# Optimization experiments

Hardware: AMD Instinct MI355X
Metric: run time of the kernel (lower is better)

Reference implementation:

```python
import jax, jax.numpy as jnp
import numpy as np

N, C, H, W = 8, 256, 128, 128
HD = 256          # hidden_depth
FC, FS, CS = 8, 2, 8  # heads_count, fold_size, center_size
EPS_GN = 1e-5


def setup_inputs() -> dict:
    key = jax.random.key(0)
    ks = jax.random.split(key, 8)
    d = {
        'x': jax.random.normal(ks[0], (N, C, H, W), jnp.float32),
        'proj_w': jax.random.normal(ks[1], (2 * HD, C), jnp.float32) * 0.02,
        'proj_b': jnp.zeros((2 * HD,), jnp.float32),
        'merge_w': jax.random.normal(ks[2], (C, HD), jnp.float32) * 0.02,
        'merge_b': jnp.zeros((C,), jnp.float32),
        'alpha': jnp.ones((1,), jnp.float32),
        'beta': jnp.zeros((1,), jnp.float32),
        'g0_w': jnp.ones((C,), jnp.float32),
        'g0_b': jnp.zeros((C,), jnp.float32),
        'mlp_w0': jax.random.normal(ks[3], (2 * C, 2 * C), jnp.float32) * 0.02,
        'mlp_b0': jnp.zeros((2 * C,), jnp.float32),
        'mlp_w1': jax.random.normal(ks[4], (2 * C, C), jnp.float32) * 0.02,
        'mlp_b1': jnp.zeros((C,), jnp.float32),
        'g1_w': jnp.ones((C,), jnp.float32),
        'g1_b': jnp.zeros((C,), jnp.float32),
        'layer_scale': jnp.full((C,), 1e-5, jnp.float32),
    }
    return d


def _group_norm1(x, w, b):
    # GroupNorm(1, C): normalize over (C,H,W) per sample, per-channel affine
    mu = x.mean(axis=(1, 2, 3), keepdims=True)
    var = ((x - mu) ** 2).mean(axis=(1, 2, 3), keepdims=True)
    xn = (x - mu) * jax.lax.rsqrt(var + EPS_GN)
    return xn * w[None, :, None, None] + b[None, :, None, None]


def _l2norm(v):
    return v / jnp.maximum(jnp.linalg.norm(v, axis=-1, keepdims=True), 1e-12)


def _local_cluster(x, proj_w, proj_b, merge_w, merge_b, alpha, beta):
    n = x.shape[0]
    # 1x1 conv proj: C -> 2*HD
    y = jnp.einsum('nchw,oc->nohw', x, proj_w) + proj_b[None, :, None, None]
    c = y.shape[1] // FC              # per-head channels (2*HD/FC)
    h, w = H // FS, W // FS
    # 'n (fc c) (fh h) (fw w) -> (n fc fh fw) c h w'
    y = y.reshape(n, FC, c, FS, h, FS, w).transpose(0, 1, 3, 5, 2, 4, 6)
    y = y.reshape(n * FC * FS * FS, c, h, w)
    m = y.shape[0]
    # adaptive avg pool to CSxCS (h,w divisible by CS -> uniform pooling)
    center = y.reshape(m, c, CS, h // CS, CS, w // CS).mean(axis=(3, 5))
    L, s = h * w, CS * CS
    yf = y.reshape(m, c, L).transpose(0, 2, 1)       # [m, L, c]
    cf = center.reshape(m, c, s).transpose(0, 2, 1)  # [m, s, c]
    cv = c // 2
    x_point, x_value = yf[..., :cv], yf[..., cv:]
    c_point, c_value = cf[..., :cv], cf[..., cv:]
    sim = jnp.einsum('mlc,msc->mls', _l2norm(x_point), _l2norm(c_point))
    sim = jax.nn.sigmoid(alpha * sim + beta)         # [m, L, s]
    vals = sim.max(axis=2)                           # [m, L]
    idx = sim.argmax(axis=2) + s * jnp.arange(m)[:, None]
    vals = vals.reshape(-1)
    idx = idx.reshape(-1)
    xv = x_value.reshape(-1, cv)
    cvv = c_value.reshape(-1, cv)
    xv_aug = jnp.concatenate([xv, jnp.ones((xv.shape[0], 1), xv.dtype)], axis=1)
    cv_aug = jnp.concatenate([cvv, jnp.ones((cvv.shape[0], 1), cvv.dtype)], axis=1)
    # scatter-add weighted points into centers
    nc = cv_aug.at[idx].add(vals[:, None] * xv_aug)
    nc = nc[:, :-1] / nc[:, -1:]
    # gather back
    nx = vals[:, None] * nc[idx]                     # [m*L, cv]
    # '(n fc fh fw h w) c -> n (fc c) (fh h) (fw w)'
    nx = nx.reshape(n, FC, FS, FS, h, w, cv).transpose(0, 1, 6, 2, 4, 3, 5)
    nx = nx.reshape(n, FC * cv, H, W)                # [n, HD, H, W]
    return jnp.einsum('nchw,oc->nohw', nx, merge_w) + merge_b[None, :, None, None]


def reference(x, proj_w, proj_b, merge_w, merge_b, alpha, beta, g0_w, g0_b,
              mlp_w0, mlp_b0, mlp_w1, mlp_b1, g1_w, g1_b, layer_scale):
    new_x = _local_cluster(x, proj_w, proj_b, merge_w, merge_b, alpha, beta)
    new_x = _group_norm1(new_x, g0_w, g0_b)
    t = jnp.concatenate([x, new_x], axis=1)          # [n, 2C, H, W]
    t = t.transpose(0, 2, 3, 1)                      # NHWC
    t = jax.nn.gelu(t @ mlp_w0 + mlp_b0, approximate=False)
    t = t @ mlp_w1 + mlp_b1
    t = t.transpose(0, 3, 1, 2)                      # NCHW
    t = _group_norm1(t, g1_w, g1_b)
    t = t * layer_scale[None, :, None, None]
    return t + x
```

## Files before the change

### kernel.cpp

```cpp
#include <hip/hip_runtime.h>
#include <math.h>

#define PIX   16384
#define NB    8
#define CIN   256

typedef __attribute__((ext_vector_type(8))) short    short8;
typedef __attribute__((ext_vector_type(4))) float    f32x4;
typedef __attribute__((ext_vector_type(4))) unsigned short us4;
typedef __attribute__((ext_vector_type(8))) unsigned short us8;

__device__ __forceinline__ float bf2f(unsigned short h) {
  return __uint_as_float(((unsigned int)h) << 16);
}
__device__ __forceinline__ unsigned short f2bf(float f) {
  unsigned int u = __float_as_uint(f);
  return (unsigned short)((u + 0x7FFFu + ((u >> 16) & 1u)) >> 16);
}
__device__ __forceinline__ float gelu_f(float v) {
  return 0.5f * v * (1.f + erff(v * 0.70710678118654752f));
}

__global__ void zero_kernel(float* p, int n) {
  int i = blockIdx.x * blockDim.x + threadIdx.x;
  if (i < n) p[i] = 0.f;
}

__global__ void prep_weights(const float* __restrict__ pw_f, const float* __restrict__ mw_f,
                             const float* __restrict__ w0, const float* __restrict__ w1,
                             unsigned short* __restrict__ pw, unsigned short* __restrict__ mw,
                             unsigned short* __restrict__ w0t, unsigned short* __restrict__ w1t) {
  const int S1 = 512 * 256, S2 = 256 * 256, S3 = 512 * 512, S4 = 256 * 512;
  int i = blockIdx.x * 256 + threadIdx.x;
  if (i < S1) { pw[i] = f2bf(pw_f[i]); return; }
  i -= S1;
  if (i < S2) { mw[i] = f2bf(mw_f[i]); return; }
  i -= S2;
  if (i < S3) { int o = i >> 9, k = i & 511; w0t[i] = f2bf(w0[k * 512 + o]); return; }
  i -= S3;
  if (i < S4) { int o = i >> 9, k = i & 511; w1t[i] = f2bf(w1[k * 256 + o]); }
}

__global__ __launch_bounds__(256) void x_to_nhwc(const float* __restrict__ x,
                                                 unsigned short* __restrict__ xT) {
  __shared__ float tile[64][65];
  const int t = threadIdx.x;
  const int p0 = blockIdx.x * 64, c0 = blockIdx.y * 64, n = blockIdx.z;
#pragma unroll
  for (int i = 0; i < 4; i++) {
    const int c = i * 16 + (t >> 4);
    const float4 v = *(const float4*)(x + ((size_t)(n * 256 + c0 + c) << 14) + p0 + (t & 15) * 4);
    tile[c][(t & 15) * 4]     = v.x;
    tile[c][(t & 15) * 4 + 1] = v.y;
    tile[c][(t & 15) * 4 + 2] = v.z;
    tile[c][(t & 15) * 4 + 3] = v.w;
  }
  __syncthreads();
#pragma unroll
  for (int i = 0; i < 4; i++) {
    const int pp = i * 16 + (t >> 4);
    const int cl = (t & 15) * 4;
    us4 o;
    o.x = f2bf(tile[cl][pp]); o.y = f2bf(tile[cl + 1][pp]);
    o.z = f2bf(tile[cl + 2][pp]); o.w = f2bf(tile[cl + 3][pp]);
    *(us4*)&xT[(((size_t)n << 14) + p0 + pp) * 256 + c0 + cl] = o;
  }
}

template<bool CONCAT, bool GELU, bool STATS>
__global__ __launch_bounds__(256, 2) void mfma_gemm(
    const unsigned short* __restrict__ A, const float* __restrict__ bias,
    const unsigned short* __restrict__ B1, const unsigned short* __restrict__ B2,
    unsigned short* __restrict__ Y, int M, int K, int K1,
    int astride, int bstride, float* __restrict__ sums) {
  __shared__ unsigned short As[8192];
  __shared__ unsigned short Bs[8192];
  __shared__ float r1[4], r2[4];
  const int t = threadIdx.x;
  const int lane = t & 63, w = t >> 6;
  const int quad = lane >> 4, l16 = lane & 15;
  const int p0 = blockIdx.x * 128, m0 = blockIdx.y * 128;
  const int n = blockIdx.z;
  const int wm = w & 1, wn = w >> 1;
  const int K2 = K - K1;

  A += (size_t)n * astride;

  f32x4 acc[4][4];
#pragma unroll
  for (int im = 0; im < 4; im++)
#pragma unroll
    for (int in = 0; in < 4; in++) acc[im][in] = (f32x4)0.f;

  for (int k0 = 0; k0 < K; k0 += 64) {
    __syncthreads();
#pragma unroll
    for (int i = 0; i < 4; i++) {
      const int c = (w << 2) | i;
      const int tm = c >> 1, kk = c & 1;
      const int krow = k0 + kk * 32 + quad * 8;
      const unsigned short* ga = A + (size_t)(m0 + tm * 16 + l16) * K + krow;
      __builtin_amdgcn_global_load_lds((const __attribute__((address_space(1))) void*)ga,
          (__attribute__((address_space(3))) void*)&As[c * 512], 16, 0, 0);
      const int prow = p0 + tm * 16 + l16;
      const unsigned short* gb;
      if (!CONCAT || krow < K1)
        gb = B1 + ((((size_t)n << 14) + prow) * (size_t)K1) + krow;
      else
        gb = B2 + ((((size_t)n << 14) + prow) * (size_t)K2) + (krow - K1);
      __builtin_amdgcn_global_load_lds((const __attribute__((address_space(1))) void*)gb,
          (__attribute__((address_space(3))) void*)&Bs[c * 512], 16, 0, 0);
    }
    __syncthreads();
#pragma unroll
    for (int kk = 0; kk < 2; kk++) {
      short8 af[4], bfr[4];
#pragma unroll
      for (int im = 0; im < 4; im++)
        af[im] = *(const short8*)&As[(((wm * 4 + im) * 2 + kk) * 64 + lane) * 8];
#pragma unroll
      for (int in = 0; in < 4; in++)
        bfr[in] = *(const short8*)&Bs[(((wn * 4 + in) * 2 + kk) * 64 + lane) * 8];
#pragma unroll
      for (int im = 0; im < 4; im++)
#pragma unroll
        for (int in = 0; in < 4; in++)
          acc[im][in] = __builtin_amdgcn_mfma_f32_16x16x32_bf16(af[im], bfr[in], acc[im][in], 0, 0, 0);
    }
  }

  const size_t nb = ((size_t)n << 14);
  float s = 0.f, s2 = 0.f;
#pragma unroll
  for (int im = 0; im < 4; im++) {
    const int om = m0 + (wm * 4 + im) * 16 + quad * 4;
    const f32x4 bv = *(const f32x4*)(bias + (size_t)n * bstride + om);
#pragma unroll
    for (int in = 0; in < 4; in++) {
      const int p = p0 + (wn * 4 + in) * 16 + l16;
      float v0 = acc[im][in].x + bv.x;
      float v1 = acc[im][in].y + bv.y;
      float v2 = acc[im][in].z + bv.z;
      float v3 = acc[im][in].w + bv.w;
      if (GELU) { v0 = gelu_f(v0); v1 = gelu_f(v1); v2 = gelu_f(v2); v3 = gelu_f(v3); }
      if (STATS) {
        s += (v0 + v1) + (v2 + v3);
        s2 = fmaf(v0, v0, s2); s2 = fmaf(v1, v1, s2);
        s2 = fmaf(v2, v2, s2); s2 = fmaf(v3, v3, s2);
      }
      us4 o4;
      o4.x = f2bf(v0); o4.y = f2bf(v1); o4.z = f2bf(v2); o4.w = f2bf(v3);
      *(us4*)&Y[(nb + p) * M + om] = o4;
    }
  }
  if (STATS) {
#pragma unroll
    for (int off = 32; off > 0; off >>= 1) {
      s += __shfl_down(s, off);
      s2 += __shfl_down(s2, off);
    }
    if (lane == 0) { r1[w] = s; r2[w] = s2; }
    __syncthreads();
    if (t == 0) {
      atomicAdd(&sums[2 * n],     (r1[0] + r1[1]) + (r1[2] + r1[3]));
      atomicAdd(&sums[2 * n + 1], (r2[0] + r2[1]) + (r2[2] + r2[3]));
    }
  }
}

__global__ __launch_bounds__(1024) void cluster_kernel(
    const unsigned short* __restrict__ y, const float* __restrict__ alpha_p,
    const float* __restrict__ beta_p, unsigned short* __restrict__ nx) {
  const int m = blockIdx.x;
  const int n = m >> 5, f = (m >> 2) & 7, s1 = (m >> 1) & 1, s2 = m & 1;
  const int t = threadIdx.x;
  const int wave = t >> 6, lane = t & 63;
  const int quad = lane >> 4, l16 = lane & 15;
  const float alpha = alpha_p[0], beta = beta_p[0];

  __shared__ float cs[64][68];
  __shared__ unsigned short cpnh[64][32];
  __shared__ float accv[64][36];
  __shared__ float svals[4096];
  __shared__ unsigned char sbest[4096];

  const size_t nbase = ((size_t)n << 14);
  const int prow0 = s1 * 64, pcol0 = s2 * 64;
  const int ch0 = f * 64;

  {
    const int b = t >> 4, g = t & 15;
    const int pr0 = prow0 + (b >> 3) * 8, pc0 = pcol0 + (b & 7) * 8;
    float a4[4] = {0.f, 0.f, 0.f, 0.f};
#pragma unroll 1
    for (int r = 0; r < 8; r++) {
#pragma unroll
      for (int cc = 0; cc < 8; cc++) {
        const us4 v = *(const us4*)(y + (nbase + (size_t)(pr0 + r) * 128 + pc0 + cc) * 512 + ch0 + g * 4);
        a4[0] += bf2f(v.x); a4[1] += bf2f(v.y); a4[2] += bf2f(v.z); a4[3] += bf2f(v.w);
      }
    }
#pragma unroll
    for (int j = 0; j < 4; j++) cs[b][g * 4 + j] = a4[j] * (1.f / 64.f);
  }
  __syncthreads();

  if (t < 64) {
    const int b = t;
    float s = 0.f;
#pragma unroll
    for (int cc = 0; cc < 32; cc++) { float v = cs[b][cc]; s = fmaf(v, v, s); }
    const float inv = 1.f / fmaxf(sqrtf(s), 1e-12f);
#pragma unroll
    for (int cc = 0; cc < 32; cc++) cpnh[b][cc] = f2bf(cs[b][cc] * inv);
#pragma unroll
    for (int q = 0; q < 32; q++) accv[b][q] = cs[b][32 + q];
    accv[b][32] = 1.f;
  }
  __syncthreads();

#pragma unroll 1
  for (int tile = 0; tile < 16; tile++) {
    const int pidx = wave * 256 + tile * 16;
    const int pix = (prow0 + (pidx >> 6)) * 128 + pcol0 + (pidx & 63) + l16;
    const unsigned short* yp = y + (nbase + pix) * 512 + ch0;
    const short8 apt = *(const short8*)(yp + quad * 8);
    const short8 avl = *(const short8*)(yp + 32 + quad * 8);

    float nrm = 0.f;
#pragma unroll
    for (int j = 0; j < 8; j++) {
      const float fv = bf2f((unsigned short)apt[j]);
      nrm = fmaf(fv, fv, nrm);
    }
    nrm += __shfl_xor(nrm, 16);
    nrm += __shfl_xor(nrm, 32);
    const float inva = 1.f / fmaxf(sqrtf(nrm), 1e-12f);

    f32x4 d[4];
#pragma unroll
    for (int g = 0; g < 4; g++) {
      const short8 bfr = *(const short8*)&cpnh[g * 16 + l16][quad * 8];
      d[g] = __builtin_amdgcn_mfma_f32_16x16x32_bf16(apt, bfr, (f32x4)0.f, 0, 0, 0);
    }

    float bv[4]; int bi[4];
#pragma unroll
    for (int r = 0; r < 4; r++) {
      bv[r] = d[0][r]; bi[r] = l16;
#pragma unroll
      for (int g = 1; g < 4; g++) {
        const float c = d[g][r];
        if (c > bv[r]) { bv[r] = c; bi[r] = g * 16 + l16; }
      }
    }
#pragma unroll
    for (int r = 0; r < 4; r++) {
#pragma unroll
      for (int msk = 1; msk < 16; msk <<= 1) {
        const float v2 = __shfl_xor(bv[r], msk);
        const int   i2 = __shfl_xor(bi[r], msk);
        if (v2 > bv[r] || (v2 == bv[r] && i2 < bi[r])) { bv[r] = v2; bi[r] = i2; }
      }
    }
    const float rv01 = (l16 & 1) ? bv[1] : bv[0];
    const float rv23 = (l16 & 1) ? bv[3] : bv[2];
    const float rowv = (l16 & 2) ? rv23 : rv01;
    const int   ri01 = (l16 & 1) ? bi[1] : bi[0];
    const int   ri23 = (l16 & 1) ? bi[3] : bi[2];
    const int   rowi = (l16 & 2) ? ri23 : ri01;
    const int sl4 = (((l16 >> 2) << 4) | (l16 & 3)) << 2;
    const float dot = __int_as_float(__builtin_amdgcn_ds_bpermute(sl4, __float_as_int(rowv)));
    const int   idx = __builtin_amdgcn_ds_bpermute(sl4, rowi);

    const float val = 1.f / (1.f + __expf(-fmaf(alpha, dot * inva, beta)));
    if (quad == 0) {
      svals[pidx + l16] = val;
      sbest[pidx + l16] = (unsigned char)idx;
    }
#pragma unroll
    for (int j = 0; j < 8; j++)
      atomicAdd(&accv[idx][quad * 8 + j], val * bf2f((unsigned short)avl[j]));
    if (quad == 0) atomicAdd(&accv[idx][32], val);
  }
  __syncthreads();

  for (int i = t; i < 2048; i += 1024) {
    const int b = i >> 5, q = i & 31;
    accv[b][q] = accv[b][q] / accv[b][32];
  }
  __syncthreads();

#pragma unroll
  for (int i = 0; i < 4; i++) {
    const int l = i * 1024 + t;
    const int p = (prow0 + (l >> 6)) * 128 + pcol0 + (l & 63);
    const float v = svals[l];
    const int b = sbest[l];
    unsigned short* nr = nx + (nbase + p) * 256 + f * 32;
#pragma unroll
    for (int q8 = 0; q8 < 4; q8++) {
      us8 o;
#pragma unroll
      for (int j = 0; j < 8; j++) o[j] = f2bf(v * accv[b][q8 * 8 + j]);
      *(us8*)&nr[q8 * 8] = o;
    }
  }
}

__global__ void gn_finalize0(const float* __restrict__ sums, const float* __restrict__ g0w,
                             const float* __restrict__ g0b, float* __restrict__ scl,
                             float* __restrict__ bia) {
  const int n = blockIdx.x, c = threadIdx.x;
  const float cntinv = 1.f / (float)(CIN * PIX);
  const float mu = sums[2 * n] * cntinv;
  const float var = sums[2 * n + 1] * cntinv - mu * mu;
  const float rs = rsqrtf(var + 1e-5f);
  const float a = rs * g0w[c];
  scl[n * 256 + c] = a;
  bia[n * 256 + c] = g0b[c] - mu * a;
}

__global__ void w0_scale(const unsigned short* __restrict__ w0t,
                         const float* __restrict__ scl, unsigned short* __restrict__ w0s) {
  const int n = blockIdx.y;
  const int i = blockIdx.x * 256 + threadIdx.x;
  const int k = i & 511;
  unsigned short v = w0t[i];
  if (k >= 256) v = f2bf(bf2f(v) * scl[n * 256 + k - 256]);
  w0s[(size_t)n * 262144 + i] = v;
}

__global__ void b0_eff(const unsigned short* __restrict__ w0t, const float* __restrict__ b0,
                       const float* __restrict__ bia, float* __restrict__ b0e) {
  const int n = blockIdx.y;
  const int o = blockIdx.x * 256 + threadIdx.x;
  float s = b0[o];
  const unsigned short* wr = w0t + (size_t)o * 512 + 256;
  const float* br = bia + n * 256;
#pragma unroll 4
  for (int k = 0; k < 256; k++) s = fmaf(bf2f(wr[k]), br[k], s);
  b0e[n * 512 + o] = s;
}

__global__ __launch_bounds__(256) void final_transpose(
    const unsigned short* __restrict__ u, const float* __restrict__ x,
    const float* __restrict__ sums, const float* __restrict__ g1w,
    const float* __restrict__ g1b, const float* __restrict__ lsc,
    float* __restrict__ out) {
  __shared__ float tile[64][68];
  const int t = threadIdx.x;
  const int p0 = blockIdx.x * 64, c0 = blockIdx.y * 64, n = blockIdx.z;
  {
    const int pl = t >> 2, g = t & 3;
    const unsigned short* up = u + ((((size_t)n << 14) + p0 + pl) << 8) + c0 + g * 16;
    const us8 v0 = *(const us8*)up;
    const us8 v1 = *(const us8*)(up + 8);
#pragma unroll
    for (int j = 0; j < 8; j++) {
      tile[pl][g * 16 + j] = bf2f(v0[j]);
      tile[pl][g * 16 + 8 + j] = bf2f(v1[j]);
    }
  }
  __syncthreads();
  {
    const int cl = t >> 2, g = t & 3;
    const int c = c0 + cl;
    const float cntinv = 1.f / (float)(CIN * PIX);
    const float mu = sums[2 * n] * cntinv;
    const float var = sums[2 * n + 1] * cntinv - mu * mu;
    const float rs = rsqrtf(var + 1e-5f);
    const float gw = rs * g1w[c] * lsc[c];
    const float gb = (g1b[c] - mu * rs * g1w[c]) * lsc[c];
    const size_t rowb = ((size_t)(n * 256 + c) << 14) + p0 + g * 16;
#pragma unroll
    for (int q = 0; q < 4; q++) {
      const float4 xv = *(const float4*)(x + rowb + q * 4);
      float4 o;
      o.x = fmaf(tile[g * 16 + q * 4][cl], gw, gb) + xv.x;
      o.y = fmaf(tile[g * 16 + q * 4 + 1][cl], gw, gb) + xv.y;
      o.z = fmaf(tile[g * 16 + q * 4 + 2][cl], gw, gb) + xv.z;
      o.w = fmaf(tile[g * 16 + q * 4 + 3][cl], gw, gb) + xv.w;
      *(float4*)(out + rowb + q * 4) = o;
    }
  }
}

extern "C" void kernel_launch(void* const* d_in, const int* in_sizes, int n_in,
                              void* d_out, int out_size, void* d_ws, size_t ws_size,
                              hipStream_t stream) {
  const float* x       = (const float*)d_in[0];
  const float* proj_w  = (const float*)d_in[1];
  const float* proj_b  = (const float*)d_in[2];
  const float* merge_w = (const float*)d_in[3];
  const float* merge_b = (const float*)d_in[4];
  const float* alpha   = (const float*)d_in[5];
  const float* beta    = (const float*)d_in[6];
  const float* g0w     = (const float*)d_in[7];
  const float* g0b     = (const float*)d_in[8];
  const float* w0      = (const float*)d_in[9];
  const float* b0      = (const float*)d_in[10];
  const float* w1      = (const float*)d_in[11];
  const float* b1      = (const float*)d_in[12];
  const float* g1w     = (const float*)d_in[13];
  const float* g1b     = (const float*)d_in[14];
  const float* lsc     = (const float*)d_in[15];
  float* out = (float*)d_out;

  unsigned short* wsu = (unsigned short*)d_ws;
  unsigned short* xT  = wsu;
  unsigned short* y   = xT + (size_t)33554432;
  unsigned short* nx  = y + (size_t)67108864;
  unsigned short* pw  = nx + (size_t)33554432;
  unsigned short* mw  = pw + 131072;
  unsigned short* w0t = mw + 65536;
  unsigned short* w1t = w0t + 262144;
  unsigned short* w0s = w1t + 131072;
  float* sums = (float*)(w0s + (size_t)2097152);
  float* scl0 = sums + 32;
  float* bia0 = scl0 + 2048;
  float* b0e  = bia0 + 2048;
  unsigned short* newx = (unsigned short*)d_out;

  zero_kernel<<<1, 64, 0, stream>>>(sums, 32);
  prep_weights<<<2304, 256, 0, stream>>>(proj_w, merge_w, w0, w1, pw, mw, w0t, w1t);
  x_to_nhwc<<<dim3(256, 4, NB), 256, 0, stream>>>(x, xT);

  mfma_gemm<false, false, false><<<dim3(128, 4, NB), 256, 0, stream>>>(
      pw, proj_b, xT, nullptr, y, 512, 256, 256, 0, 0, nullptr);

  cluster_kernel<<<256, 1024, 0, stream>>>(y, alpha, beta, nx);

  mfma_gemm<false, false, true><<<dim3(128, 2, NB), 256, 0, stream>>>(
      mw, merge_b, nx, nullptr, newx, 256, 256, 256, 0, 0, sums);

  gn_finalize0<<<NB, 256, 0, stream>>>(sums, g0w, g0b, scl0, bia0);
  w0_scale<<<dim3(1024, NB), 256, 0, stream>>>(w0t, scl0, w0s);
  b0_eff<<<dim3(2, NB), 256, 0, stream>>>(w0t, b0, bia0, b0e);

  mfma_gemm<true, true, false><<<dim3(128, 4, NB), 256, 0, stream>>>(
      w0s, b0e, xT, newx, y, 512, 512, 256, 262144, 512, nullptr);

  mfma_gemm<false, false, true><<<dim3(128, 2, NB), 256, 0, stream>>>(
      w1t, b1, y, nullptr, nx, 256, 512, 512, 0, 0, sums + 16);

  final_transpose<<<dim3(256, 4, NB), 256, 0, stream>>>(
      nx, x, sums + 16, g1w, g1b, lsc, out);
}
```

Baseline: 1.003 ms.

## Optimize cluster kernel argmax with DPP, register-prefetch tiles, hoist center fragments

Several changes to the cluster kernel. Point loads are prefetched two tiles ahead into registers, the center B-fragments are hoisted out of the tile loop, and the shuffle-based argmax is replaced by a DPP row-max plus ballot/ffs index recovery. The value and index are also packed into a single bpermute, and accv is read with vector LDS loads. The aim is to hide global load latency and cut the cross-lane shuffle cost. Packing the index into the low 6 mantissa bits slightly perturbs the dot value, and launch_bounds(1024,4) may force register spills.

```diff
diff --git a/kernel.cpp b/kernel.cpp
--- a/kernel.cpp
+++ b/kernel.cpp
@@ -19,6 +19,18 @@
 }
 __device__ __forceinline__ float gelu_f(float v) {
   return 0.5f * v * (1.f + erff(v * 0.70710678118654752f));
+}
+
+__device__ __forceinline__ float rowmax16(float v) {
+  v = fmaxf(v, __uint_as_float(__builtin_amdgcn_update_dpp(
+        __float_as_uint(v), __float_as_uint(v), 0x121, 0xF, 0xF, false)));
+  v = fmaxf(v, __uint_as_float(__builtin_amdgcn_update_dpp(
+        __float_as_uint(v), __float_as_uint(v), 0x122, 0xF, 0xF, false)));
+  v = fmaxf(v, __uint_as_float(__builtin_amdgcn_update_dpp(
+        __float_as_uint(v), __float_as_uint(v), 0x124, 0xF, 0xF, false)));
+  v = fmaxf(v, __uint_as_float(__builtin_amdgcn_update_dpp(
+        __float_as_uint(v), __float_as_uint(v), 0x128, 0xF, 0xF, false)));
+  return v;
 }
 
 __global__ void zero_kernel(float* p, int n) {
@@ -168,7 +180,7 @@
   }
 }
 
-__global__ __launch_bounds__(1024) void cluster_kernel(
+__global__ __launch_bounds__(1024, 4) void cluster_kernel(
     const unsigned short* __restrict__ y, const float* __restrict__ alpha_p,
     const float* __restrict__ beta_p, unsigned short* __restrict__ nx) {
   const int m = blockIdx.x;
@@ -219,13 +231,23 @@
   }
   __syncthreads();
 
-#pragma unroll 1
-  for (int tile = 0; tile < 16; tile++) {
+  const short8 cb0 = *(const short8*)&cpnh[ 0 + l16][quad * 8];
+  const short8 cb1 = *(const short8*)&cpnh[16 + l16][quad * 8];
+  const short8 cb2 = *(const short8*)&cpnh[32 + l16][quad * 8];
+  const short8 cb3 = *(const short8*)&cpnh[48 + l16][quad * 8];
+  const int sl4 = (((l16 >> 2) << 4) | (l16 & 3)) << 2;
+  const int sh = quad << 4;
+
+  auto loadpt = [&](int tile, short8& a, short8& v) {
     const int pidx = wave * 256 + tile * 16;
     const int pix = (prow0 + (pidx >> 6)) * 128 + pcol0 + (pidx & 63) + l16;
-    const unsigned short* yp = y + (nbase + pix) * 512 + ch0;
-    const short8 apt = *(const short8*)(yp + quad * 8);
-    const short8 avl = *(const short8*)(yp + 32 + quad * 8);
+    const unsigned short* yp = y + (nbase + pix) * 512 + ch0 + quad * 8;
+    a = *(const short8*)yp;
+    v = *(const short8*)(yp + 32);
+  };
+
+  auto compute_tile = [&](int tile, short8 apt, short8 avl) {
+    const int pidx = wave * 256 + tile * 16;
 
     float nrm = 0.f;
 #pragma unroll
@@ -237,41 +259,42 @@
     nrm += __shfl_xor(nrm, 32);
     const float inva = 1.f / fmaxf(sqrtf(nrm), 1e-12f);
 
-    f32x4 d[4];
-#pragma unroll
-    for (int g = 0; g < 4; g++) {
-      const short8 bfr = *(const short8*)&cpnh[g * 16 + l16][quad * 8];
-      d[g] = __builtin_amdgcn_mfma_f32_16x16x32_bf16(apt, bfr, (f32x4)0.f, 0, 0, 0);
-    }
+    const f32x4 d0 = __builtin_amdgcn_mfma_f32_16x16x32_bf16(apt, cb0, (f32x4)0.f, 0, 0, 0);
+    const f32x4 d1 = __builtin_amdgcn_mfma_f32_16x16x32_bf16(apt, cb1, (f32x4)0.f, 0, 0, 0);
+    const f32x4 d2 = __builtin_amdgcn_mfma_f32_16x16x32_bf16(apt, cb2, (f32x4)0.f, 0, 0, 0);
+    const f32x4 d3 = __builtin_amdgcn_mfma_f32_16x16x32_bf16(apt, cb3, (f32x4)0.f, 0, 0, 0);
 
     float bv[4]; int bi[4];
 #pragma unroll
     for (int r = 0; r < 4; r++) {
-      bv[r] = d[0][r]; bi[r] = l16;
-#pragma unroll
-      for (int g = 1; g < 4; g++) {
-        const float c = d[g][r];
-        if (c > bv[r]) { bv[r] = c; bi[r] = g * 16 + l16; }
-      }
-    }
-#pragma unroll
-    for (int r = 0; r < 4; r++) {
-#pragma unroll
-      for (int msk = 1; msk < 16; msk <<= 1) {
-        const float v2 = __shfl_xor(bv[r], msk);
-        const int   i2 = __shfl_xor(bi[r], msk);
-        if (v2 > bv[r] || (v2 == bv[r] && i2 < bi[r])) { bv[r] = v2; bi[r] = i2; }
-      }
-    }
+      float v = fmaxf(fmaxf(d0[r], d1[r]), fmaxf(d2[r], d3[r]));
+      v = rowmax16(v);
+      bv[r] = v;
+      const unsigned long long m0 = __ballot(d0[r] == v);
+      const unsigned long long m1 = __ballot(d1[r] == v);
+      const unsigned long long m2 = __ballot(d2[r] == v);
+      const unsigned long long m3 = __ballot(d3[r] == v);
+      const unsigned f0 = (unsigned)(m0 >> sh) & 0xFFFFu;
+      const unsigned f1 = (unsigned)(m1 >> sh) & 0xFFFFu;
+      const unsigned f2 = (unsigned)(m2 >> sh) & 0xFFFFu;
+      const unsigned f3 = (unsigned)(m3 >> sh) & 0xFFFFu;
+      int ii = 48 + __ffs(f3) - 1;
+      if (f2) ii = 32 + __ffs(f2) - 1;
+      if (f1) ii = 16 + __ffs(f1) - 1;
+      if (f0) ii = __ffs(f0) - 1;
+      bi[r] = ii;
+    }
+
     const float rv01 = (l16 & 1) ? bv[1] : bv[0];
     const float rv23 = (l16 & 1) ? bv[3] : bv[2];
     const float rowv = (l16 & 2) ? rv23 : rv01;
     const int   ri01 = (l16 & 1) ? bi[1] : bi[0];
     const int   ri23 = (l16 & 1) ? bi[3] : bi[2];
     const int   rowi = (l16 & 2) ? ri23 : ri01;
-    const int sl4 = (((l16 >> 2) << 4) | (l16 & 3)) << 2;
-    const float dot = __int_as_float(__builtin_amdgcn_ds_bpermute(sl4, __float_as_int(rowv)));
-    const int   idx = __builtin_amdgcn_ds_bpermute(sl4, rowi);
+    const unsigned pk = (__float_as_uint(rowv) & ~63u) | (unsigned)rowi;
+    const unsigned got = (unsigned)__builtin_amdgcn_ds_bpermute(sl4, (int)pk);
+    const int   idx = (int)(got & 63u);
+    const float dot = __uint_as_float(got & ~63u);
 
     const float val = 1.f / (1.f + __expf(-fmaf(alpha, dot * inva, beta)));
     if (quad == 0) {
@@ -282,6 +305,19 @@
     for (int j = 0; j < 8; j++)
       atomicAdd(&accv[idx][quad * 8 + j], val * bf2f((unsigned short)avl[j]));
     if (quad == 0) atomicAdd(&accv[idx][32], val);
+  };
+
+  {
+    short8 aA, vA, aB, vB;
+    short8 aC = {}, vC = {}, aD = {}, vD = {};
+    loadpt(0, aA, vA); loadpt(1, aB, vB);
+#pragma unroll 1
+    for (int tp = 0; tp < 16; tp += 2) {
+      if (tp < 14) { loadpt(tp + 2, aC, vC); loadpt(tp + 3, aD, vD); }
+      compute_tile(tp,     aA, vA);
+      compute_tile(tp + 1, aB, vB);
+      if (tp < 14) { aA = aC; vA = vC; aB = aD; vB = vD; }
+    }
   }
   __syncthreads();
 
@@ -300,9 +336,13 @@
     unsigned short* nr = nx + (nbase + p) * 256 + f * 32;
 #pragma unroll
     for (int q8 = 0; q8 < 4; q8++) {
+      const f32x4 a0 = *(const f32x4*)&accv[b][q8 * 8];
+      const f32x4 a1 = *(const f32x4*)&accv[b][q8 * 8 + 4];
       us8 o;
-#pragma unroll
-      for (int j = 0; j < 8; j++) o[j] = f2bf(v * accv[b][q8 * 8 + j]);
+      o[0] = f2bf(v * a0.x); o[1] = f2bf(v * a0.y);
+      o[2] = f2bf(v * a0.z); o[3] = f2bf(v * a0.w);
+      o[4] = f2bf(v * a1.x); o[5] = f2bf(v * a1.y);
+      o[6] = f2bf(v * a1.z); o[7] = f2bf(v * a1.w);
       *(us8*)&nr[q8 * 8] = o;
     }
   }
```

New measurement: 976.2 us. 2.6% less time.
